# Performance work log

Hardware: AMD Instinct MI355X
Metric: run time of the kernel (lower is better)

Reference implementation:

```python
import jax, jax.numpy as jnp
import numpy as np

B, N, P, E = 64, 512, 256, 4096          # batch, nodes (stations), partition nodes, edges
NUM_NWP, LP, F = 8, 16, 32               # num_nwp, local_points, local_cnn_dims
NT, ED, H, W = 8, 8, 64, 8               # num_temp, edge_feature_dims, decf_mlp_hidden, weight_function_dim
G, RH = 64, 256                          # gnn_dim, readout_hid_dim
H1, Q = 128, 9                           # mlp_hid_dim1, num quantiles


def setup_inputs() -> dict:
    key = jax.random.key(0)
    ks = iter(jax.random.split(key, 40))
    def rn(shape, s=0.05):
        return jax.random.normal(next(ks), shape, dtype=jnp.float32) * s
    # one-hot incidence matrices: each edge has one left (partition) node and one right node
    lidx = jax.random.randint(next(ks), (E,), 0, P)
    ridx = jax.random.randint(next(ks), (E,), 0, N)
    linc = jnp.zeros((P, E), jnp.float32).at[lidx, jnp.arange(E)].set(1.0)
    rinc = jnp.zeros((E, N), jnp.float32).at[jnp.arange(E), ridx].set(1.0)
    inp = {
        "x1": jax.random.normal(next(ks), (B, NUM_NWP * N, LP), dtype=jnp.float32),
        "x2": jax.random.normal(next(ks), (B, NT), dtype=jnp.float32),
        # LocalConv1D grouped conv (torch OIW layout: [Cout, Cin/groups, K])
        "conv_w": rn((F * N, NUM_NWP, LP)), "conv_b": rn((F * N,)),
        # WDSGCN2 edge-weight MLP
        "k1_w": rn((H, ED)), "k1_b": rn((H,)),
        "k2_w": rn((H, NT)),
        "k3_w": rn((H, F)),
        "k4_w": rn((H, F)),
        "k5_w": rn((W, H)), "k5_b": rn((W,)),
        "gc_w": rn((G, F * W)), "gc_b": rn((G,)),
        # readout
        "r0_w": rn((RH, G * P)),
        "r1_w": rn((RH, NT)), "r1_b": rn((RH,)),
        "r2_w": rn((RH, P)),
        "r3_w": rn((P, RH)), "r3_b": rn((P,)),
        # SMlp (forward uses l1 -> ELU -> l3 only)
        "l1_w": rn((H1, NT + G)), "l1_b": rn((H1,)),
        "l3_w": rn((Q, H1)), "l3_b": rn((Q,)),
        # buffers
        "ef": jax.random.normal(next(ks), (E, ED + 1), dtype=jnp.float32),
        "linc": linc,
        "rinc": rinc,
        "cap_feature": jax.random.normal(next(ks), (P,), dtype=jnp.float32),
        "partition_idx": jnp.arange(P, dtype=jnp.int32) * (N // P),
    }
    return inp


def reference(x1, x2, conv_w, conv_b, k1_w, k1_b, k2_w, k3_w, k4_w, k5_w, k5_b,
              gc_w, gc_b, r0_w, r1_w, r1_b, r2_w, r3_w, r3_b,
              l1_w, l1_b, l3_w, l3_b, ef, linc, rinc, cap_feature, partition_idx):
    b = x1.shape[0]
    # --- LocalConv1D: grouped conv1d (valid padding, output length 1) + ReLU ---
    y = jax.lax.conv_general_dilated(x1, conv_w, (1,), 'VALID',
                                     dimension_numbers=('NCH', 'OIH', 'NCH'),
                                     feature_group_count=N)
    x = jax.nn.relu(y + conv_b[None, :, None]).reshape(b, N, F)      # [B,N,F]
    # --- WDSGCN2: per-edge weight kernel ---
    kern = ef[:, :-1] @ k1_w.T + k1_b                                # [E,H]
    kern = kern[None] + (x2 @ k2_w.T)[:, None, :]                    # [B,E,H]
    xp = x[:, partition_idx, :]                                      # [B,P,F]
    kern = kern + jnp.einsum('pe,bpf->bef', linc, xp) @ k3_w.T       # left-node feats
    rx = jnp.einsum('en,bnf->bef', rinc, x)                          # right-node feats [B,E,F]
    kern = kern + rx @ k4_w.T
    kern = jax.nn.relu(jax.nn.leaky_relu(kern, 0.02) @ k5_w.T + k5_b)  # [B,E,W]
    # --- message = kernel (outer) right-node features, aggregated by left incidence ---
    msg = kern[:, :, :, None] * rx[:, :, None, :]                    # [B,E,W,F]
    agg = jnp.einsum('pe,bewf->bpwf', linc, msg).reshape(b, P, W * F)
    yg = jax.nn.relu(agg @ gc_w.T + gc_b)                            # [B,P,G]
    # --- readout attention over partition nodes ---
    h = yg.reshape(b, -1) @ r0_w.T + (x2 @ r1_w.T + r1_b) + cap_feature @ r2_w.T
    wt = jax.nn.relu(jax.nn.leaky_relu(h, 0.01) @ r3_w.T + r3_b)     # [B,P]
    res = jnp.einsum('bp,bpg->bg', wt, yg)                           # [B,G]
    # --- SMlp head ---
    z = jnp.concatenate([res, x2], axis=1)
    z = jax.nn.elu(z @ l1_w.T + l1_b)
    return z @ l3_w.T + l3_b                                         # [B,Q]
```

## Files before the change

### kernel.cpp

```cpp
#include <hip/hip_runtime.h>
#include <math.h>

#define B_ 64
#define N_ 512
#define P_ 256
#define E_ 4096
#define F_ 32
#define H_ 64
#define W_ 8
#define G_ 64
#define RH_ 256

#define X_OFF   0
#define T4_OFF  (X_OFF + N_*B_*F_)
#define T3_OFF  (T4_OFF + N_*B_*H_)
#define KB_OFF  (T3_OFF + P_*B_*H_)
#define KW_OFF  (KB_OFF + E_*H_)
#define YG_OFF  (KW_OFF + E_*B_*W_)
#define HB_OFF  (YG_OFF + B_*P_*G_)
#define RES_OFF (HB_OFF + B_*RH_)
#define INT_OFF (RES_OFF + 4*B_*G_)

__device__ __forceinline__ unsigned short f2bf(float f) {
  unsigned int u = __float_as_uint(f);
  u = u + 0x7fffu + ((u >> 16) & 1u);
  return (unsigned short)(u >> 16);
}

__global__ __launch_bounds__(256) void k_dc(
    const float* __restrict__ linc, const float* __restrict__ rinc,
    int* __restrict__ lidx, int* __restrict__ ridx,
    const float* __restrict__ x1, const float* __restrict__ conv_w,
    const float* __restrict__ conv_b, float* __restrict__ x,
    unsigned short* __restrict__ xh) {
  __shared__ float wsm[32 * 132];
  __shared__ float xsm[8192];
  int blk = blockIdx.x, t = threadIdx.x;
  if (blk < 3072) {
    int i4 = blk * 256 + t;
    const int L4 = (P_ * E_) / 4;
    if (i4 < L4) {
      float4 v = ((const float4*)linc)[i4];
      int i = i4 * 4;
      int p = i >> 12, e = i & 4095;
      if (v.x != 0.0f) lidx[e]     = p;
      if (v.y != 0.0f) lidx[e + 1] = p;
      if (v.z != 0.0f) lidx[e + 2] = p;
      if (v.w != 0.0f) lidx[e + 3] = p;
    } else {
      int j4 = i4 - L4;
      float4 v = ((const float4*)rinc)[j4];
      int j = j4 * 4;
      int e = j >> 9, n = j & 511;
      if (v.x != 0.0f) ridx[e] = n;
      if (v.y != 0.0f) ridx[e] = n + 1;
      if (v.z != 0.0f) ridx[e] = n + 2;
      if (v.w != 0.0f) ridx[e] = n + 3;
    }
    return;
  }
  int n = blk - 3072;
  for (int i = t; i < 1024; i += 256) {
    int f = i >> 5, j = i & 31;
    ((float4*)wsm)[f * 33 + j] = ((const float4*)(conv_w + n * 4096))[i];
  }
  for (int i = t; i < 2048; i += 256) {
    int b = i >> 5, j = i & 31;
    ((float4*)xsm)[i] = ((const float4*)(x1 + b * 65536 + n * 128))[j];
  }
  __syncthreads();
  int f = t & 31, bq = t >> 5;
  float cb = conv_b[n * 32 + f];
  float acc[8];
#pragma unroll
  for (int bi = 0; bi < 8; bi++) acc[bi] = cb;
  const float4* wf4 = (const float4*)wsm + f * 33;
  const float4* xb4 = (const float4*)xsm + bq * 256;
#pragma unroll 4
  for (int k4 = 0; k4 < 32; k4++) {
    float4 wv = wf4[k4];
#pragma unroll
    for (int bi = 0; bi < 8; bi++) {
      float4 xv = xb4[bi * 32 + k4];
      acc[bi] += wv.x * xv.x + wv.y * xv.y + wv.z * xv.z + wv.w * xv.w;
    }
  }
#pragma unroll
  for (int bi = 0; bi < 8; bi++) {
    int b = bq * 8 + bi;
    float vv = fmaxf(acc[bi], 0.0f);
    x[n * 2048 + b * 32 + f] = vv;
    xh[n * 2048 + b * 32 + f] = f2bf(vv);
  }
}

__global__ __launch_bounds__(256) void k_prep(
    const float* __restrict__ x, const int* __restrict__ pidx,
    const float* __restrict__ k3_w, const float* __restrict__ k4_w,
    const float* __restrict__ x2, const float* __restrict__ k2_w,
    const float* __restrict__ ef, const float* __restrict__ k1_w,
    const float* __restrict__ k1_b,
    const float* __restrict__ r1_w, const float* __restrict__ r1_b,
    const float* __restrict__ r2_w, const float* __restrict__ cap,
    const int* __restrict__ lidx, const int* __restrict__ ridx,
    unsigned short* __restrict__ t4h, float* __restrict__ t3,
    float* __restrict__ kb, float* __restrict__ hbuf,
    int* __restrict__ part_start, int2* __restrict__ pe2) {
  __shared__ float xsh[2048];
  __shared__ float wsh[64 * 36];
  __shared__ float x2s[512];
  __shared__ float k2s[512];
  __shared__ int cnt[256];
  __shared__ int buf[256];
  __shared__ int cur[256];
  int blk = blockIdx.x, t = threadIdx.x;
  if (blk < 768) {
    bool isT4 = blk < 512;
    int n = isT4 ? blk : pidx[blk - 512];
    const float* wmat = isT4 ? k4_w : k3_w;
    float* outp = t3 + (isT4 ? 0 : (blk - 512) * 4096);
    for (int i = t; i < 512; i += 256) {
      ((float4*)xsh)[i] = ((const float4*)(x + n * 2048))[i];
      int h = i >> 3, j = i & 7;
      ((float4*)wsh)[h * 9 + j] = ((const float4*)wmat)[i];
    }
    if (isT4) {
      for (int i = t; i < 128; i += 256) {
        ((float4*)x2s)[i] = ((const float4*)x2)[i];
        ((float4*)k2s)[i] = ((const float4*)k2_w)[i];
      }
    }
    __syncthreads();
    int h = t & 63, bq = t >> 6;
    float wreg[32];
#pragma unroll
    for (int j = 0; j < 8; j++) {
      float4 v = ((float4*)wsh)[h * 9 + j];
      wreg[4 * j] = v.x; wreg[4 * j + 1] = v.y; wreg[4 * j + 2] = v.z; wreg[4 * j + 3] = v.w;
    }
    float w2[8];
    if (isT4) {
      float4 u = ((float4*)k2s)[h * 2], v = ((float4*)k2s)[h * 2 + 1];
      w2[0] = u.x; w2[1] = u.y; w2[2] = u.z; w2[3] = u.w;
      w2[4] = v.x; w2[5] = v.y; w2[6] = v.z; w2[7] = v.w;
    }
    for (int bi = 0; bi < 16; bi++) {
      int b = bq * 16 + bi;
      float acc = 0.0f;
#pragma unroll
      for (int j = 0; j < 8; j++) {
        float4 xv = ((float4*)xsh)[b * 8 + j];
        acc += xv.x * wreg[4 * j] + xv.y * wreg[4 * j + 1] +
               xv.z * wreg[4 * j + 2] + xv.w * wreg[4 * j + 3];
      }
      if (isT4) {
        float4 u = ((float4*)x2s)[b * 2], v = ((float4*)x2s)[b * 2 + 1];
        acc += u.x * w2[0] + u.y * w2[1] + u.z * w2[2] + u.w * w2[3] +
               v.x * w2[4] + v.y * w2[5] + v.z * w2[6] + v.w * w2[7];
        t4h[blk * 4096 + b * 64 + h] = f2bf(acc);
      } else {
        outp[b * 64 + h] = acc;
      }
    }
  } else if (blk < 1792) {
    int o = (blk - 768) * 256 + t;
    int e = o >> 6, h = o & 63;
    float acc = k1_b[h];
    const float* er = ef + e * 9;
    const float* kr = k1_w + h * 8;
#pragma unroll
    for (int d = 0; d < 8; d++) acc += er[d] * kr[d];
    kb[o] = acc;
  } else if (blk < 1856) {
    int o = (blk - 1792) * 256 + t;
    int rh = o & 255;
    float acc = r1_b[rh];
    const float* xr = x2 + (o >> 8) * 8;
    const float* rr = r1_w + rh * 8;
#pragma unroll
    for (int d = 0; d < 8; d++) acc += xr[d] * rr[d];
    const float* r2r = r2_w + rh * 256;
    for (int p4 = 0; p4 < 64; p4++) {
      float4 cv = ((const float4*)cap)[p4];
      float4 rv = ((const float4*)r2r)[p4];
      acc += cv.x * rv.x + cv.y * rv.y + cv.z * rv.z + cv.w * rv.w;
    }
    hbuf[o] = acc;
  } else {
    cnt[t] = 0;
    __syncthreads();
    for (int e = t; e < E_; e += 256) atomicAdd(&cnt[lidx[e]], 1);
    __syncthreads();
    buf[t] = cnt[t];
    __syncthreads();
    for (int off = 1; off < 256; off <<= 1) {
      int add = (t >= off) ? buf[t - off] : 0;
      __syncthreads();
      buf[t] += add;
      __syncthreads();
    }
    part_start[t + 1] = buf[t];
    if (t == 0) part_start[0] = 0;
    cur[t] = buf[t] - cnt[t];
    __syncthreads();
    for (int e = t; e < E_; e += 256) {
      int p = lidx[e];
      int pos = atomicAdd(&cur[p], 1);
      pe2[pos] = make_int2(e | (p << 16), ridx[e]);
    }
  }
}

__global__ __launch_bounds__(256) void k_kern(
    const float* __restrict__ kb, const float* __restrict__ t3,
    const unsigned short* __restrict__ t4h, const float* __restrict__ k5_w,
    const float* __restrict__ k5_b, const int2* __restrict__ pe2,
    float* __restrict__ kv) {
  __shared__ float k5t[4 * 520];
  int bid = blockIdx.x;
  int pos = (bid & 7) * 512 + (bid >> 3);
  int t = threadIdx.x;
  for (int i = t; i < 512; i += 256) {
    int h = i >> 3, w = i & 7;
    float v = k5_w[w * 64 + h];
#pragma unroll
    for (int qq = 0; qq < 4; qq++) k5t[qq * 520 + i] = v;
  }
  int2 c = pe2[pos];
  int e = c.x & 0xffff, p = c.x >> 16, r = c.y;
  int s = t & 3, b = t >> 2;
  __syncthreads();
  const float* kq = k5t + s * 520 + s * 128;
  const float4* kb4 = (const float4*)(kb + e * 64 + s * 16);
  const float4* t34 = (const float4*)(t3 + p * 4096 + b * 64 + s * 16);
  const int4* t4p = (const int4*)(t4h + r * 4096 + b * 64 + s * 16);
  int4 ta = t4p[0], tb = t4p[1];
  float t4v[16];
  {
    unsigned int uu;
    uu = (unsigned int)ta.x; t4v[0]  = __uint_as_float(uu << 16); t4v[1]  = __uint_as_float(uu & 0xffff0000u);
    uu = (unsigned int)ta.y; t4v[2]  = __uint_as_float(uu << 16); t4v[3]  = __uint_as_float(uu & 0xffff0000u);
    uu = (unsigned int)ta.z; t4v[4]  = __uint_as_float(uu << 16); t4v[5]  = __uint_as_float(uu & 0xffff0000u);
    uu = (unsigned int)ta.w; t4v[6]  = __uint_as_float(uu << 16); t4v[7]  = __uint_as_float(uu & 0xffff0000u);
    uu = (unsigned int)tb.x; t4v[8]  = __uint_as_float(uu << 16); t4v[9]  = __uint_as_float(uu & 0xffff0000u);
    uu = (unsigned int)tb.y; t4v[10] = __uint_as_float(uu << 16); t4v[11] = __uint_as_float(uu & 0xffff0000u);
    uu = (unsigned int)tb.z; t4v[12] = __uint_as_float(uu << 16); t4v[13] = __uint_as_float(uu & 0xffff0000u);
    uu = (unsigned int)tb.w; t4v[14] = __uint_as_float(uu << 16); t4v[15] = __uint_as_float(uu & 0xffff0000u);
  }
  float lk[16];
#pragma unroll
  for (int j4 = 0; j4 < 4; j4++) {
    float4 a = kb4[j4], cc = t34[j4];
    float v;
    v = a.x + cc.x + t4v[j4 * 4 + 0]; lk[j4 * 4 + 0] = v > 0.0f ? v : 0.02f * v;
    v = a.y + cc.y + t4v[j4 * 4 + 1]; lk[j4 * 4 + 1] = v > 0.0f ? v : 0.02f * v;
    v = a.z + cc.z + t4v[j4 * 4 + 2]; lk[j4 * 4 + 2] = v > 0.0f ? v : 0.02f * v;
    v = a.w + cc.w + t4v[j4 * 4 + 3]; lk[j4 * 4 + 3] = v > 0.0f ? v : 0.02f * v;
  }
  float pw[8] = {0, 0, 0, 0, 0, 0, 0, 0};
#pragma unroll
  for (int j = 0; j < 16; j++) {
    float4 u = *(const float4*)(kq + j * 8);
    float4 v = *(const float4*)(kq + j * 8 + 4);
    float l = lk[j];
    pw[0] += l * u.x; pw[1] += l * u.y; pw[2] += l * u.z; pw[3] += l * u.w;
    pw[4] += l * v.x; pw[5] += l * v.y; pw[6] += l * v.z; pw[7] += l * v.w;
  }
#pragma unroll
  for (int w = 0; w < 8; w++) {
    pw[w] += __shfl_xor(pw[w], 1);
    pw[w] += __shfl_xor(pw[w], 2);
  }
  float2 o;
  o.x = fmaxf(pw[2 * s] + k5_b[2 * s], 0.0f);
  o.y = fmaxf(pw[2 * s + 1] + k5_b[2 * s + 1], 0.0f);
  *(float2*)(kv + pos * 512 + b * 8 + 2 * s) = o;
}

__global__ __launch_bounds__(512, 2) void k_agg(
    const unsigned short* __restrict__ xh, const float* __restrict__ kv,
    const int2* __restrict__ pe2, const int* __restrict__ part_start,
    const float* __restrict__ gc_w, const float* __restrict__ gc_b,
    float* __restrict__ yg) {
  __shared__ float accS[64 * 128];
  __shared__ float gcS[64 * 256];
  int p = blockIdx.x, t = threadIdx.x;
  int slot = t >> 8;
  int ts = t & 255;
  int s = ts & 3, b = ts >> 2;
  for (int i4 = t; i4 < 4096; i4 += 512)
    ((float4*)gcS)[i4] = ((const float4*)gc_w)[i4];
  float acc[64];
#pragma unroll
  for (int j = 0; j < 64; j++) acc[j] = 0.0f;
  int s0 = part_start[p], s1 = part_start[p + 1];
  int idx = s0 + slot;
  int r = (idx < s1) ? pe2[idx].y : 0;
  for (; idx < s1; idx += 2) {
    int rn = (idx + 2 < s1) ? pe2[idx + 2].y : 0;
    const float4* kvp = (const float4*)(kv + idx * 512 + b * 8);
    float4 ka = kvp[0], kc = kvp[1];
    int4 xw = *(const int4*)(xh + r * 2048 + b * 32 + s * 8);
    float kw[8] = {ka.x, ka.y, ka.z, ka.w, kc.x, kc.y, kc.z, kc.w};
    float xa[8];
    {
      unsigned int uu;
      uu = (unsigned int)xw.x; xa[0] = __uint_as_float(uu << 16); xa[1] = __uint_as_float(uu & 0xffff0000u);
      uu = (unsigned int)xw.y; xa[2] = __uint_as_float(uu << 16); xa[3] = __uint_as_float(uu & 0xffff0000u);
      uu = (unsigned int)xw.z; xa[4] = __uint_as_float(uu << 16); xa[5] = __uint_as_float(uu & 0xffff0000u);
      uu = (unsigned int)xw.w; xa[6] = __uint_as_float(uu << 16); xa[7] = __uint_as_float(uu & 0xffff0000u);
    }
#pragma unroll
    for (int w = 0; w < 8; w++)
#pragma unroll
      for (int j = 0; j < 8; j++) acc[w * 8 + j] += kw[w] * xa[j];
    r = rn;
  }
  int gq = t >> 6, be = t & 63;
  float ac[8];
#pragma unroll
  for (int i = 0; i < 8; i++) ac[i] = 0.0f;
#pragma unroll
  for (int ph = 0; ph < 2; ph++) {
    if (ph) __syncthreads();
    if (slot == 0) {
#pragma unroll
      for (int w2 = 0; w2 < 4; w2++)
#pragma unroll
        for (int j4 = 0; j4 < 2; j4++) {
          int khalf4 = w2 * 8 + s * 2 + j4;
          int phys4 = (khalf4 & 24) | ((khalf4 ^ b) & 7);
          int j = (ph * 4 + w2) * 8 + j4 * 4;
          *(float4*)(accS + b * 128 + phys4 * 4) =
              make_float4(acc[j], acc[j + 1], acc[j + 2], acc[j + 3]);
        }
    }
    __syncthreads();
    if (slot == 1) {
#pragma unroll
      for (int w2 = 0; w2 < 4; w2++)
#pragma unroll
        for (int j4 = 0; j4 < 2; j4++) {
          int khalf4 = w2 * 8 + s * 2 + j4;
          int phys4 = (khalf4 & 24) | ((khalf4 ^ b) & 7);
          int j = (ph * 4 + w2) * 8 + j4 * 4;
          float4* ptr = (float4*)(accS + b * 128 + phys4 * 4);
          float4 o = *ptr;
          o.x += acc[j]; o.y += acc[j + 1]; o.z += acc[j + 2]; o.w += acc[j + 3];
          *ptr = o;
        }
    }
    __syncthreads();
    for (int k4h = 0; k4h < 32; k4h++) {
      int phys4 = (k4h & 24) | ((k4h ^ be) & 7);
      float4 av = *(const float4*)(accS + be * 128 + phys4 * 4);
      int w2 = k4h >> 3;
      int k4g = (ph * 4 + w2) * 8 + (k4h & 7);
#pragma unroll
      for (int i = 0; i < 8; i++) {
        float4 wv = *(const float4*)(gcS + (gq * 8 + i) * 256 + k4g * 4);
        ac[i] += av.x * wv.x + av.y * wv.y + av.z * wv.z + av.w * wv.w;
      }
    }
  }
  float* yp = yg + be * 16384 + p * 64 + gq * 8;
#pragma unroll
  for (int i = 0; i < 8; i++)
    yp[i] = fmaxf(ac[i] + gc_b[gq * 8 + i], 0.0f);
}

__global__ __launch_bounds__(256) void k_r0(const float* __restrict__ yg,
    const float* __restrict__ r0_w, float* __restrict__ part) {
  __shared__ float ygs[64 * 68];
  __shared__ float wts[64 * 260];
  int kc = blockIdx.x, t = threadIdx.x;
  int k0 = kc * 64;
  {
    int c = t >> 4, rr = t & 15;
    for (int rd = 0; rd < 16; rd++) {
      int rh = rd * 16 + rr;
      float4 v = *(const float4*)(r0_w + rh * 16384 + k0 + c * 4);
      wts[(4 * c + 0) * 260 + rh] = v.x;
      wts[(4 * c + 1) * 260 + rh] = v.y;
      wts[(4 * c + 2) * 260 + rh] = v.z;
      wts[(4 * c + 3) * 260 + rh] = v.w;
    }
  }
  {
    int b = t >> 2, kq = t & 3;
    const float* src = yg + b * 16384 + k0 + kq * 16;
#pragma unroll
    for (int u = 0; u < 4; u++) {
      float4 v = *(const float4*)(src + u * 4);
      int kk = kq * 16 + u * 4;
      ygs[(kk + 0) * 68 + b] = v.x;
      ygs[(kk + 1) * 68 + b] = v.y;
      ygs[(kk + 2) * 68 + b] = v.z;
      ygs[(kk + 3) * 68 + b] = v.w;
    }
  }
  __syncthreads();
  int lane = t & 63, wv = t >> 6;
  int b8 = lane & 7, r8 = lane >> 3;
  const float* yp = ygs + b8 * 8;
  const float* wp = wts + wv * 64 + r8 * 8;
  float acc[8][8];
#pragma unroll
  for (int i = 0; i < 8; i++)
#pragma unroll
    for (int j = 0; j < 8; j++) acc[i][j] = 0.0f;
#pragma unroll 2
  for (int k = 0; k < 64; k++) {
    float4 ya = *(const float4*)(yp + k * 68);
    float4 yb = *(const float4*)(yp + k * 68 + 4);
    float4 wa = *(const float4*)(wp + k * 260);
    float4 wb = *(const float4*)(wp + k * 260 + 4);
    float yv[8] = {ya.x, ya.y, ya.z, ya.w, yb.x, yb.y, yb.z, yb.w};
    float wr[8] = {wa.x, wa.y, wa.z, wa.w, wb.x, wb.y, wb.z, wb.w};
#pragma unroll
    for (int i = 0; i < 8; i++)
#pragma unroll
      for (int j = 0; j < 8; j++) acc[i][j] += yv[i] * wr[j];
  }
  float* pb = part + kc * 16384 + wv * 64 + r8 * 8;
#pragma unroll
  for (int i = 0; i < 8; i++) {
    float4 s0 = make_float4(acc[i][0], acc[i][1], acc[i][2], acc[i][3]);
    float4 s1 = make_float4(acc[i][4], acc[i][5], acc[i][6], acc[i][7]);
    float* pp = pb + (b8 * 8 + i) * 256;
    *(float4*)pp = s0;
    *(float4*)(pp + 4) = s1;
  }
}

__global__ __launch_bounds__(256) void k_r0red(const float* __restrict__ part,
    float* __restrict__ hbuf) {
  int blk = blockIdx.x;
  int oq = blk & 63, kq = blk >> 6;
  int o = oq * 256 + threadIdx.x;
  float s = 0.0f;
  const float* pp = part + kq * 64 * 16384 + o;
#pragma unroll 8
  for (int kc = 0; kc < 64; kc++) s += pp[kc * 16384];
  atomicAdd(&hbuf[o], s);
}

__global__ __launch_bounds__(256) void k_wt_res(const float* __restrict__ hbuf,
    const float* __restrict__ r3_w, const float* __restrict__ r3_b,
    const float* __restrict__ yg, float* __restrict__ res4) {
  __shared__ float hs[256];
  __shared__ float wts[64];
  __shared__ float red[256];
  int blk = blockIdx.x;
  int bb = blk >> 2, pq = blk & 3;
  int t = threadIdx.x;
  float hv = hbuf[bb * 256 + t];
  hs[t] = hv > 0.0f ? hv : 0.01f * hv;
  __syncthreads();
  int pl = t >> 2, c = t & 3;
  int pp = pq * 64 + pl;
  const float4* wrow = (const float4*)(r3_w + pp * 256 + c * 64);
  const float4* h4 = (const float4*)(hs) + c * 16;
  float a = 0.0f;
#pragma unroll
  for (int j = 0; j < 16; j++) {
    float4 w4 = wrow[j], hh = h4[j];
    a += hh.x * w4.x + hh.y * w4.y + hh.z * w4.z + hh.w * w4.w;
  }
  a += __shfl_xor(a, 1);
  a += __shfl_xor(a, 2);
  if (c == 0) wts[pl] = fmaxf(a + r3_b[pp], 0.0f);
  __syncthreads();
  int g = t & 63, ch = t >> 6;
  float r = 0.0f;
  const float* ygp = yg + bb * 16384 + pq * 4096 + g;
#pragma unroll
  for (int pi = 0; pi < 16; pi++) {
    int pl2 = ch * 16 + pi;
    r += wts[pl2] * ygp[pl2 * 64];
  }
  red[t] = r;
  __syncthreads();
  if (t < 64)
    res4[pq * 4096 + bb * 64 + t] = red[t] + red[t + 64] + red[t + 128] + red[t + 192];
}

__global__ __launch_bounds__(128) void k_final(const float* __restrict__ res4,
    const float* __restrict__ x2, const float* __restrict__ l1_w,
    const float* __restrict__ l1_b, const float* __restrict__ l3_w,
    const float* __restrict__ l3_b, float* __restrict__ out) {
  __shared__ float zs[128];
  int bb = blockIdx.x, t = threadIdx.x;
  float acc = l1_b[t];
  const float* wrow = l1_w + t * 72;
  const float* rr = res4 + bb * 64;
#pragma unroll 8
  for (int j = 0; j < 64; j++) {
    float rv = rr[j] + rr[4096 + j] + rr[8192 + j] + rr[12288 + j];
    acc += rv * wrow[j];
  }
  const float* xr = x2 + bb * 8;
#pragma unroll
  for (int j = 0; j < 8; j++) acc += xr[j] * wrow[64 + j];
  zs[t] = acc > 0.0f ? acc : expm1f(acc);
  __syncthreads();
  if (t < 9) {
    float o = l3_b[t];
    const float* w3 = l3_w + t * 128;
    for (int j = 0; j < 128; j++) o += zs[j] * w3[j];
    out[bb * 9 + t] = o;
  }
}

extern "C" void kernel_launch(void* const* d_in, const int* in_sizes, int n_in,
                              void* d_out, int out_size, void* d_ws, size_t ws_size,
                              hipStream_t stream) {
  (void)in_sizes; (void)n_in; (void)out_size; (void)ws_size;
  const float* x1     = (const float*)d_in[0];
  const float* x2     = (const float*)d_in[1];
  const float* conv_w = (const float*)d_in[2];
  const float* conv_b = (const float*)d_in[3];
  const float* k1_w   = (const float*)d_in[4];
  const float* k1_b   = (const float*)d_in[5];
  const float* k2_w   = (const float*)d_in[6];
  const float* k3_w   = (const float*)d_in[7];
  const float* k4_w   = (const float*)d_in[8];
  const float* k5_w   = (const float*)d_in[9];
  const float* k5_b   = (const float*)d_in[10];
  const float* gc_w   = (const float*)d_in[11];
  const float* gc_b   = (const float*)d_in[12];
  const float* r0_w   = (const float*)d_in[13];
  const float* r1_w   = (const float*)d_in[14];
  const float* r1_b   = (const float*)d_in[15];
  const float* r2_w   = (const float*)d_in[16];
  const float* r3_w   = (const float*)d_in[17];
  const float* r3_b   = (const float*)d_in[18];
  const float* l1_w   = (const float*)d_in[19];
  const float* l1_b   = (const float*)d_in[20];
  const float* l3_w   = (const float*)d_in[21];
  const float* l3_b   = (const float*)d_in[22];
  const float* ef     = (const float*)d_in[23];
  const float* linc   = (const float*)d_in[24];
  const float* rinc   = (const float*)d_in[25];
  const float* cap    = (const float*)d_in[26];
  const int*   pidx   = (const int*)d_in[27];
  float* out = (float*)d_out;

  float* ws   = (float*)d_ws;
  float* xbuf = ws + X_OFF;
  unsigned short* t4h = (unsigned short*)(ws + T4_OFF);
  unsigned short* xh  = (unsigned short*)(ws + T4_OFF + N_*B_*H_/2);
  float* t3   = ws + T3_OFF;
  float* kb   = ws + KB_OFF;
  float* kv   = ws + KW_OFF;
  float* yg   = ws + YG_OFF;
  float* hbuf = ws + HB_OFF;
  float* res4 = ws + RES_OFF;
  float* part = ws + X_OFF;
  int* ib = (int*)(ws + INT_OFF);
  int* lidx = ib;
  int* ridx = ib + 4096;
  int* part_start = ib + 8192;
  int2* pe2 = (int2*)(ib + 8704);

  hipLaunchKernelGGL(k_dc, dim3(3584), dim3(256), 0, stream,
                     linc, rinc, lidx, ridx, x1, conv_w, conv_b, xbuf, xh);
  hipLaunchKernelGGL(k_prep, dim3(1857), dim3(256), 0, stream,
                     xbuf, pidx, k3_w, k4_w, x2, k2_w, ef, k1_w, k1_b,
                     r1_w, r1_b, r2_w, cap, lidx, ridx,
                     t4h, t3, kb, hbuf, part_start, pe2);
  hipLaunchKernelGGL(k_kern, dim3(4096), dim3(256), 0, stream,
                     kb, t3, t4h, k5_w, k5_b, pe2, kv);
  hipLaunchKernelGGL(k_agg, dim3(256), dim3(512), 0, stream,
                     xh, kv, pe2, part_start, gc_w, gc_b, yg);
  hipLaunchKernelGGL(k_r0, dim3(256), dim3(256), 0, stream, yg, r0_w, part);
  hipLaunchKernelGGL(k_r0red, dim3(256), dim3(256), 0, stream, part, hbuf);
  hipLaunchKernelGGL(k_wt_res, dim3(256), dim3(256), 0, stream, hbuf, r3_w, r3_b, yg, res4);
  hipLaunchKernelGGL(k_final, dim3(64), dim3(128), 0, stream,
                     res4, x2, l1_w, l1_b, l3_w, l3_b, out);
}
```

Before: 237.3 us.

## Retile r0 GEMM split-K with rh quarters and hoist cap·r2 matvec

```diff
diff --git a/kernel.cpp b/kernel.cpp
--- a/kernel.cpp
+++ b/kernel.cpp
@@ -32,7 +32,9 @@
     int* __restrict__ lidx, int* __restrict__ ridx,
     const float* __restrict__ x1, const float* __restrict__ conv_w,
     const float* __restrict__ conv_b, float* __restrict__ x,
-    unsigned short* __restrict__ xh) {
+    unsigned short* __restrict__ xh,
+    const float* __restrict__ cap, const float* __restrict__ r2_w,
+    float* __restrict__ capv) {
   __shared__ float wsm[32 * 132];
   __shared__ float xsm[8192];
   int blk = blockIdx.x, t = threadIdx.x;
@@ -59,6 +61,17 @@
     }
     return;
   }
+  if (blk == 3584) {
+    float acc = 0.0f;
+    const float* rr = r2_w + t * 256;
+    for (int p4 = 0; p4 < 64; p4++) {
+      float4 cv = ((const float4*)cap)[p4];
+      float4 rv = ((const float4*)rr)[p4];
+      acc += cv.x * rv.x + cv.y * rv.y + cv.z * rv.z + cv.w * rv.w;
+    }
+    capv[t] = acc;
+    return;
+  }
   int n = blk - 3072;
   for (int i = t; i < 1024; i += 256) {
     int f = i >> 5, j = i & 31;
@@ -101,7 +114,7 @@
     const float* __restrict__ ef, const float* __restrict__ k1_w,
     const float* __restrict__ k1_b,
     const float* __restrict__ r1_w, const float* __restrict__ r1_b,
-    const float* __restrict__ r2_w, const float* __restrict__ cap,
+    const float* __restrict__ capv,
     const int* __restrict__ lidx, const int* __restrict__ ridx,
     unsigned short* __restrict__ t4h, float* __restrict__ t3,
     float* __restrict__ kb, float* __restrict__ hbuf,
@@ -174,17 +187,11 @@
   } else if (blk < 1856) {
     int o = (blk - 1792) * 256 + t;
     int rh = o & 255;
-    float acc = r1_b[rh];
+    float acc = r1_b[rh] + capv[rh];
     const float* xr = x2 + (o >> 8) * 8;
     const float* rr = r1_w + rh * 8;
 #pragma unroll
     for (int d = 0; d < 8; d++) acc += xr[d] * rr[d];
-    const float* r2r = r2_w + rh * 256;
-    for (int p4 = 0; p4 < 64; p4++) {
-      float4 cv = ((const float4*)cap)[p4];
-      float4 rv = ((const float4*)r2r)[p4];
-      acc += cv.x * rv.x + cv.y * rv.y + cv.z * rv.z + cv.w * rv.w;
-    }
     hbuf[o] = acc;
   } else {
     cnt[t] = 0;
@@ -372,64 +379,68 @@
 __global__ __launch_bounds__(256) void k_r0(const float* __restrict__ yg,
     const float* __restrict__ r0_w, float* __restrict__ part) {
   __shared__ float ygs[64 * 68];
-  __shared__ float wts[64 * 260];
-  int kc = blockIdx.x, t = threadIdx.x;
-  int k0 = kc * 64;
-  {
-    int c = t >> 4, rr = t & 15;
-    for (int rd = 0; rd < 16; rd++) {
-      int rh = rd * 16 + rr;
-      float4 v = *(const float4*)(r0_w + rh * 16384 + k0 + c * 4);
-      wts[(4 * c + 0) * 260 + rh] = v.x;
-      wts[(4 * c + 1) * 260 + rh] = v.y;
-      wts[(4 * c + 2) * 260 + rh] = v.z;
-      wts[(4 * c + 3) * 260 + rh] = v.w;
-    }
-  }
-  {
-    int b = t >> 2, kq = t & 3;
-    const float* src = yg + b * 16384 + k0 + kq * 16;
-#pragma unroll
-    for (int u = 0; u < 4; u++) {
-      float4 v = *(const float4*)(src + u * 4);
-      int kk = kq * 16 + u * 4;
-      ygs[(kk + 0) * 68 + b] = v.x;
-      ygs[(kk + 1) * 68 + b] = v.y;
-      ygs[(kk + 2) * 68 + b] = v.z;
-      ygs[(kk + 3) * 68 + b] = v.w;
-    }
-  }
-  __syncthreads();
+  __shared__ float wts[64 * 68];
+  int bid = blockIdx.x, t = threadIdx.x;
+  int kc = ((bid >> 5) << 3) | (bid & 7);
+  int rhq = (bid >> 3) & 3;
+  int rh0 = rhq * 64;
   int lane = t & 63, wv = t >> 6;
-  int b8 = lane & 7, r8 = lane >> 3;
-  const float* yp = ygs + b8 * 8;
-  const float* wp = wts + wv * 64 + r8 * 8;
-  float acc[8][8];
-#pragma unroll
-  for (int i = 0; i < 8; i++)
-#pragma unroll
-    for (int j = 0; j < 8; j++) acc[i][j] = 0.0f;
-#pragma unroll 2
-  for (int k = 0; k < 64; k++) {
-    float4 ya = *(const float4*)(yp + k * 68);
-    float4 yb = *(const float4*)(yp + k * 68 + 4);
-    float4 wa = *(const float4*)(wp + k * 260);
-    float4 wb = *(const float4*)(wp + k * 260 + 4);
-    float yv[8] = {ya.x, ya.y, ya.z, ya.w, yb.x, yb.y, yb.z, yb.w};
-    float wr[8] = {wa.x, wa.y, wa.z, wa.w, wb.x, wb.y, wb.z, wb.w};
-#pragma unroll
-    for (int i = 0; i < 8; i++)
-#pragma unroll
-      for (int j = 0; j < 8; j++) acc[i][j] += yv[i] * wr[j];
-  }
-  float* pb = part + kc * 16384 + wv * 64 + r8 * 8;
-#pragma unroll
-  for (int i = 0; i < 8; i++) {
-    float4 s0 = make_float4(acc[i][0], acc[i][1], acc[i][2], acc[i][3]);
-    float4 s1 = make_float4(acc[i][4], acc[i][5], acc[i][6], acc[i][7]);
-    float* pp = pb + (b8 * 8 + i) * 256;
-    *(float4*)pp = s0;
-    *(float4*)(pp + 4) = s1;
+  int b4 = lane & 15;
+  int r4 = (lane >> 4) | (wv << 2);
+  float acc[4][4];
+#pragma unroll
+  for (int i = 0; i < 4; i++)
+#pragma unroll
+    for (int j = 0; j < 4; j++) acc[i][j] = 0.0f;
+  for (int sub = 0; sub < 4; sub++) {
+    int k0 = kc * 256 + sub * 64;
+    if (sub) __syncthreads();
+    {
+      int rl = t >> 2, kq = t & 3;
+      const float* src = r0_w + (rh0 + rl) * 16384 + k0 + kq * 16;
+#pragma unroll
+      for (int u = 0; u < 4; u++) {
+        float4 v = *(const float4*)(src + u * 4);
+        int kk = kq * 16 + u * 4;
+        wts[(kk + 0) * 68 + rl] = v.x;
+        wts[(kk + 1) * 68 + rl] = v.y;
+        wts[(kk + 2) * 68 + rl] = v.z;
+        wts[(kk + 3) * 68 + rl] = v.w;
+      }
+    }
+    {
+      int b = t >> 2, kq = t & 3;
+      const float* src = yg + b * 16384 + k0 + kq * 16;
+#pragma unroll
+      for (int u = 0; u < 4; u++) {
+        float4 v = *(const float4*)(src + u * 4);
+        int kk = kq * 16 + u * 4;
+        ygs[(kk + 0) * 68 + b] = v.x;
+        ygs[(kk + 1) * 68 + b] = v.y;
+        ygs[(kk + 2) * 68 + b] = v.z;
+        ygs[(kk + 3) * 68 + b] = v.w;
+      }
+    }
+    __syncthreads();
+    const float* yp = ygs + b4 * 4;
+    const float* wp = wts + r4 * 4;
+#pragma unroll 4
+    for (int k = 0; k < 64; k++) {
+      float4 yv = *(const float4*)(yp + k * 68);
+      float4 wr = *(const float4*)(wp + k * 68);
+      float ya[4] = {yv.x, yv.y, yv.z, yv.w};
+      float wa[4] = {wr.x, wr.y, wr.z, wr.w};
+#pragma unroll
+      for (int i = 0; i < 4; i++)
+#pragma unroll
+        for (int j = 0; j < 4; j++) acc[i][j] += ya[i] * wa[j];
+    }
+  }
+  float* pb = part + kc * 16384 + rh0 + r4 * 4;
+#pragma unroll
+  for (int i = 0; i < 4; i++) {
+    *(float4*)(pb + (b4 * 4 + i) * 256) =
+        make_float4(acc[i][0], acc[i][1], acc[i][2], acc[i][3]);
   }
 }
 
@@ -439,9 +450,9 @@
   int oq = blk & 63, kq = blk >> 6;
   int o = oq * 256 + threadIdx.x;
   float s = 0.0f;
-  const float* pp = part + kq * 64 * 16384 + o;
+  const float* pp = part + kq * 16 * 16384 + o;
 #pragma unroll 8
-  for (int kc = 0; kc < 64; kc++) s += pp[kc * 16384];
+  for (int kc = 0; kc < 16; kc++) s += pp[kc * 16384];
   atomicAdd(&hbuf[o], s);
 }
 
@@ -562,12 +573,14 @@
   int* ridx = ib + 4096;
   int* part_start = ib + 8192;
   int2* pe2 = (int2*)(ib + 8704);
-
-  hipLaunchKernelGGL(k_dc, dim3(3584), dim3(256), 0, stream,
-                     linc, rinc, lidx, ridx, x1, conv_w, conv_b, xbuf, xh);
+  float* capv = ws + INT_OFF + 16896;
+
+  hipLaunchKernelGGL(k_dc, dim3(3585), dim3(256), 0, stream,
+                     linc, rinc, lidx, ridx, x1, conv_w, conv_b, xbuf, xh,
+                     cap, r2_w, capv);
   hipLaunchKernelGGL(k_prep, dim3(1857), dim3(256), 0, stream,
                      xbuf, pidx, k3_w, k4_w, x2, k2_w, ef, k1_w, k1_b,
-                     r1_w, r1_b, r2_w, cap, lidx, ridx,
+                     r1_w, r1_b, capv, lidx, ridx,
                      t4h, t3, kb, hbuf, part_start, pe2);
   hipLaunchKernelGGL(k_kern, dim3(4096), dim3(256), 0, stream,
                      kb, t3, t4h, k5_w, k5_b, pe2, kv);
```

New measurement: 229.2 us. 1.04x faster.
